# Kernel optimization log

Hardware: AMD Instinct MI355X
Metric: run time of the kernel (lower is better)

## Reference

```python
import jax, jax.numpy as jnp
import numpy as np

N_ENT, N_REL, N_TRIG, N_ARGS = 100000, 250000, 50000, 250000
ENT_DIM, REL_R, RTYPE_DIM, ROLE_DIM, REL_SIZE = 288, 256, 32, 256, 200
ARG_DIM = REL_R + RTYPE_DIM + ENT_DIM  # 576


def setup_inputs() -> dict:
    key = jax.random.key(0)
    ks = jax.random.split(key, 11)
    s_in = 1.0 / np.sqrt(ARG_DIM)
    return {
        "ent_embeds": jax.random.normal(ks[0], (N_ENT, ENT_DIM), jnp.float32),
        "rel_embeds": jax.random.normal(ks[1], (N_REL, REL_R), jnp.float32),
        "rtype_table": jax.random.normal(ks[2], (REL_SIZE + 1, RTYPE_DIM), jnp.float32),
        "W_in": jax.random.normal(ks[3], (ARG_DIM, ROLE_DIM), jnp.float32) * s_in,
        "W_out": jax.random.normal(ks[4], (ARG_DIM, ROLE_DIM), jnp.float32) * s_in,
        "rtype_ids": jax.random.randint(ks[5], (N_REL,), 0, REL_SIZE, jnp.int32),
        "trig_ent_id": jax.random.randint(ks[6], (N_TRIG,), 0, N_ENT, jnp.int32),
        "arg_trig": jax.random.randint(ks[7], (N_ARGS,), 0, N_TRIG, jnp.int32),
        "arg_rel": jax.random.randint(ks[8], (N_ARGS,), 0, N_REL, jnp.int32),
        "arg_ent": jax.random.randint(ks[9], (N_ARGS,), 0, N_ENT, jnp.int32),
        "arg_is_in": jax.random.randint(ks[10], (N_ARGS,), 0, 2, jnp.int32),
    }


def reference(ent_embeds, rel_embeds, rtype_table, W_in, W_out,
              rtype_ids, trig_ent_id, arg_trig, arg_rel, arg_ent, arg_is_in):
    # per-relation type embedding (rtype_embedding_layer)
    rt_embeds = rtype_table[rtype_ids]                       # [N_REL, RTYPE_DIM]
    # per-argument gather + concat (get_arg_embeds): [rel | rtype | arg-entity]
    x = jnp.concatenate([rel_embeds[arg_rel],
                         rt_embeds[arg_rel],
                         ent_embeds[arg_ent]], axis=-1)      # [N_ARGS, ARG_DIM]
    # in_arg_layer vs out_arg_layer selected per argument (io_ids membership)
    m = arg_is_in.astype(x.dtype)[:, None]
    y = (x * m) @ W_in + (x * (1.0 - m)) @ W_out             # [N_ARGS, ROLE_DIM]
    # sum-aggregate per trigger (torch.sum over stacked arg embeds)
    args_sum = jax.ops.segment_sum(y, arg_trig, num_segments=N_TRIG)
    # concat trigger embedding with aggregated args (event_representation)
    return jnp.concatenate([ent_embeds[trig_ent_id], args_sum], axis=-1)  # [N_TRIG, ENT_DIM+ROLE_DIM]
```

## Files before the change

### kernel.cpp

```cpp
#include <hip/hip_runtime.h>
#include <hip/hip_bf16.h>
#include <stdint.h>

#define N_ENT    100000
#define N_REL    250000
#define N_TRIG   50000
#define N_ARGS   250000
#define ENT_DIM  288
#define REL_R    256
#define RTYPE_DIM 32
#define ROLE_DIM 256
#define ARG_DIM  576
#define OUT_DIM  544

#define BM 64
#define BK 32
#define NSTEP (ARG_DIM / BK)
#define LDPK 584
#define CSP 258

typedef __attribute__((ext_vector_type(8))) short bf16x8;
typedef __attribute__((ext_vector_type(4))) short bf16x4;
typedef __attribute__((ext_vector_type(4))) float f32x4;

__device__ __forceinline__ short f2b(float f) {
    union { float f; uint32_t u; } v; v.f = f;
    uint32_t u = v.u;
    uint32_t r = (u + 0x7fffu + ((u >> 16) & 1u)) >> 16;
    return (short)r;
}

__global__ void __launch_bounds__(256)
k_init(const float* __restrict__ ent, const int* __restrict__ trig_ent,
       float* __restrict__ out)
{
    const int t    = blockIdx.x * 4 + (threadIdx.x >> 6);
    const int lane = threadIdx.x & 63;
    const int e    = trig_ent[t];
    const float4* src = (const float4*)(ent + (size_t)e * ENT_DIM);
    float4*       dst = (float4*)(out + (size_t)t * OUT_DIM);
    const float4 z = {0.f, 0.f, 0.f, 0.f};
    dst[lane] = src[lane];
    if (lane < 8) dst[64 + lane] = src[64 + lane];
    dst[72 + lane] = z;
}

__global__ void __launch_bounds__(256)
k_prep_hist(const float* __restrict__ W_in, const float* __restrict__ W_out,
            short* __restrict__ Wb,
            const int* __restrict__ arg_trig, int* __restrict__ cnt)
{
    const int idx = blockIdx.x * 256 + threadIdx.x;
    {
        const int w   = idx / (ARG_DIM * ROLE_DIM);
        const int rem = idx % (ARG_DIM * ROLE_DIM);
        const int k   = rem / ROLE_DIM;
        const int col = rem % ROLE_DIM;
        const float* src = (w == 0) ? W_in : W_out;
        Wb[((size_t)w * ROLE_DIM + col) * ARG_DIM + k] = f2b(src[k * ROLE_DIM + col]);
    }
    if (idx < N_ARGS) atomicAdd(&cnt[arg_trig[idx]], 1);
}

#define SCAN_T 1024
#define SCAN_B ((N_TRIG + SCAN_T - 1) / SCAN_T)

__global__ void __launch_bounds__(SCAN_T)
k_scan1(const int* __restrict__ cnt, int* __restrict__ off,
        int* __restrict__ bsum)
{
    __shared__ int buf[SCAN_T];
    const int tid = threadIdx.x;
    const int i   = blockIdx.x * SCAN_T + tid;
    int v = (i < N_TRIG) ? cnt[i] : 0;
    buf[tid] = v;
    __syncthreads();
#pragma unroll
    for (int o = 1; o < SCAN_T; o <<= 1) {
        int x = (tid >= o) ? buf[tid - o] : 0;
        __syncthreads();
        buf[tid] += x;
        __syncthreads();
    }
    if (i < N_TRIG) off[i] = buf[tid] - v;
    if (tid == SCAN_T - 1) bsum[blockIdx.x] = buf[tid];
}

__global__ void __launch_bounds__(SCAN_T)
k_scan3(int* __restrict__ off, const int* __restrict__ bsum)
{
    __shared__ int sh;
    if (threadIdx.x == 0) {
        int s = 0;
        for (int j = 0; j < (int)blockIdx.x; ++j) s += bsum[j];
        sh = s;
    }
    __syncthreads();
    const int i = blockIdx.x * SCAN_T + threadIdx.x;
    if (i < N_TRIG) off[i] += sh;
}

__global__ void __launch_bounds__(256)
k_scatter(const int* __restrict__ arg_trig, int* __restrict__ off,
          int* __restrict__ idx)
{
    const int a = blockIdx.x * 256 + threadIdx.x;
    if (a < N_ARGS) {
        const int p = atomicAdd(&off[arg_trig[a]], 1);
        idx[p] = a;
    }
}

__global__ void __launch_bounds__(512, 4)
k_gemm(const float* __restrict__ ent,  const float* __restrict__ rel,
       const float* __restrict__ rtab, const short* __restrict__ Wb,
       const int* __restrict__ rtype_ids, const int* __restrict__ arg_trig,
       const int* __restrict__ arg_rel,   const int* __restrict__ arg_ent,
       const int* __restrict__ arg_is_in, const int* __restrict__ idx,
       float* __restrict__ out)
{
    __shared__ alignas(16) short As[BM][LDPK];
    __shared__ int s_rel[BM], s_ent[BM], s_rt[BM], s_trig[BM], s_mask[BM];

    const int tid = threadIdx.x;
    const int a0  = blockIdx.x * BM;

    if (tid < BM) {
        int i     = a0 + tid;
        int valid = (i < N_ARGS);
        int a     = idx[valid ? i : (N_ARGS - 1)];
        int r     = arg_rel[a];
        s_rel[tid]  = r;
        s_ent[tid]  = arg_ent[a];
        s_rt[tid]   = rtype_ids[r];
        s_trig[tid] = valid ? arg_trig[a] : -1;
        s_mask[tid] = valid ? arg_is_in[a] : -1;
    }
    __syncthreads();

    const int lane  = tid & 63;
    const int wave  = tid >> 6;
    const int quad  = lane >> 4;
    const int l15   = lane & 15;
    const int nbase = wave * 32;

    const int srow = tid >> 3;
    const int skq  = (tid & 7) * 4;

    const float* p_rel = rel  + (size_t)s_rel[srow] * REL_R    + skq;
    const float* p_rt  = rtab + s_rt[srow] * RTYPE_DIM         + skq;
    const float* p_ent = ent  + (size_t)s_ent[srow] * ENT_DIM  + skq;

    {
        float4 t[9];
#pragma unroll
        for (int s = 0; s < 8; ++s) t[s] = *(const float4*)(p_rel + s * BK);
        t[8] = *(const float4*)p_rt;
#pragma unroll
        for (int s = 0; s < 9; ++s) {
            bf16x4 h;
            h[0] = f2b(t[s].x); h[1] = f2b(t[s].y);
            h[2] = f2b(t[s].z); h[3] = f2b(t[s].w);
            *(bf16x4*)&As[srow][s * BK + skq] = h;
        }
    }
    {
        float4 t[9];
#pragma unroll
        for (int s = 0; s < 9; ++s) t[s] = *(const float4*)(p_ent + s * BK);
#pragma unroll
        for (int s = 0; s < 9; ++s) {
            bf16x4 h;
            h[0] = f2b(t[s].x); h[1] = f2b(t[s].y);
            h[2] = f2b(t[s].z); h[3] = f2b(t[s].w);
            *(bf16x4*)&As[srow][(s + 9) * BK + skq] = h;
        }
    }

    int rowmask[4];
#pragma unroll
    for (int m = 0; m < 4; ++m) rowmask[m] = s_mask[m * 16 + l15];

    f32x4 acc[4][2];
#pragma unroll
    for (int m = 0; m < 4; ++m)
#pragma unroll
        for (int n = 0; n < 2; ++n) acc[m][n] = (f32x4){0.f, 0.f, 0.f, 0.f};

    const short* wbl = Wb + (size_t)(nbase + l15) * ARG_DIM + quad * 8;
    const bf16x8 zf = {0, 0, 0, 0, 0, 0, 0, 0};

    __syncthreads();

#pragma unroll
    for (int s = 0; s < NSTEP; ++s) {
        const short* bp = wbl + s * BK;
        const bf16x8 bi0 = *(const bf16x8*)(bp);
        const bf16x8 bi1 = *(const bf16x8*)(bp + 16 * ARG_DIM);
        const bf16x8 bo0 = *(const bf16x8*)(bp + (size_t)ROLE_DIM * ARG_DIM);
        const bf16x8 bo1 = *(const bf16x8*)(bp + (size_t)(ROLE_DIM + 16) * ARG_DIM);

        bf16x8 a[4];
#pragma unroll
        for (int m = 0; m < 4; ++m)
            a[m] = *(const bf16x8*)&As[m * 16 + l15][s * BK + quad * 8];

#pragma unroll
        for (int m = 0; m < 4; ++m) {
            const bf16x8 ain = (rowmask[m] == 1) ? a[m] : zf;
            const bf16x8 aot = (rowmask[m] == 0) ? a[m] : zf;
            acc[m][0] = __builtin_amdgcn_mfma_f32_16x16x32_bf16(ain, bi0, acc[m][0], 0, 0, 0);
            acc[m][0] = __builtin_amdgcn_mfma_f32_16x16x32_bf16(aot, bo0, acc[m][0], 0, 0, 0);
            acc[m][1] = __builtin_amdgcn_mfma_f32_16x16x32_bf16(ain, bi1, acc[m][1], 0, 0, 0);
            acc[m][1] = __builtin_amdgcn_mfma_f32_16x16x32_bf16(aot, bo1, acc[m][1], 0, 0, 0);
        }
    }

    __syncthreads();
    float (*Cs)[CSP] = (float(*)[CSP])&As[0][0];
#pragma unroll
    for (int m = 0; m < 4; ++m)
#pragma unroll
        for (int n = 0; n < 2; ++n)
#pragma unroll
            for (int r4 = 0; r4 < 4; ++r4)
                Cs[m * 16 + quad * 4 + r4][nbase + n * 16 + l15] = acc[m][n][r4];
    __syncthreads();

    {
        const int c    = tid & 255;
        const int half = tid >> 8;
        const int r0   = half * 32;
        const int rend = r0 + 32;

        int   runTrig  = s_trig[r0];
        int   runStart = r0;
        float sum      = 0.f;
        for (int r = r0; r < rend; ++r) {
            const int t = s_trig[r];
            if (t != runTrig) {
                if (runTrig >= 0) {
                    float* p = out + (size_t)runTrig * OUT_DIM + ENT_DIM + c;
                    if (runStart == r0) atomicAdd(p, sum);
                    else                *p = sum;
                }
                runTrig = t; runStart = r; sum = 0.f;
            }
            sum += Cs[r][c];
        }
        if (runTrig >= 0) {
            float* p = out + (size_t)runTrig * OUT_DIM + ENT_DIM + c;
            atomicAdd(p, sum);
        }
    }
}

extern "C" void kernel_launch(void* const* d_in, const int* in_sizes, int n_in,
                              void* d_out, int out_size, void* d_ws, size_t ws_size,
                              hipStream_t stream)
{
    const float* ent      = (const float*)d_in[0];
    const float* rel      = (const float*)d_in[1];
    const float* rtab     = (const float*)d_in[2];
    const float* W_in     = (const float*)d_in[3];
    const float* W_out    = (const float*)d_in[4];
    const int*  rtype_ids = (const int*)d_in[5];
    const int*  trig_ent  = (const int*)d_in[6];
    const int*  arg_trig  = (const int*)d_in[7];
    const int*  arg_rel   = (const int*)d_in[8];
    const int*  arg_ent   = (const int*)d_in[9];
    const int*  arg_is_in = (const int*)d_in[10];

    float* out = (float*)d_out;

    char* ws   = (char*)d_ws;
    short* Wb  = (short*)(ws);
    int*   cnt = (int*)(ws + 589824);
    int*   off = (int*)(ws + 789824);
    int*   bsum= (int*)(ws + 989824);
    int*   idx = (int*)(ws + 990080);

    hipMemsetAsync(cnt, 0, 200000, stream);

    hipLaunchKernelGGL(k_init, dim3(N_TRIG / 4), dim3(256), 0, stream,
                       ent, trig_ent, out);
    hipLaunchKernelGGL(k_prep_hist, dim3(2 * ARG_DIM * ROLE_DIM / 256), dim3(256),
                       0, stream, W_in, W_out, Wb, arg_trig, cnt);
    hipLaunchKernelGGL(k_scan1, dim3(SCAN_B), dim3(SCAN_T), 0, stream,
                       cnt, off, bsum);
    hipLaunchKernelGGL(k_scan3, dim3(SCAN_B), dim3(SCAN_T), 0, stream,
                       off, bsum);
    hipLaunchKernelGGL(k_scatter, dim3((N_ARGS + 255) / 256), dim3(256), 0,
                       stream, arg_trig, off, idx);
    hipLaunchKernelGGL(k_gemm, dim3((N_ARGS + BM - 1) / BM), dim3(512), 0, stream,
                       ent, rel, rtab, Wb,
                       rtype_ids, arg_trig, arg_rel, arg_ent, arg_is_in, idx, out);
}
```

Before: 755.4 us.

## Pre-convert embedding tables to bf16 before gathering into GEMM tiles

Adds a conversion kernel that writes bf16 copies of the relation, entity and rtype tables into workspace. The GEMM then gathers half-width rows with 16-byte loads instead of converting fp32 rows per tile. It also switches the init copy to nontemporal stores. The aim is to cut gather bandwidth and conversion work in the GEMM, at the cost of a full-table conversion pass on every call. The new path is used only when the workspace is large enough.

```diff
diff --git a/kernel.cpp b/kernel.cpp
--- a/kernel.cpp
+++ b/kernel.cpp
@@ -12,6 +12,7 @@
 #define ROLE_DIM 256
 #define ARG_DIM  576
 #define OUT_DIM  544
+#define REL_SIZE_PLUS1 201
 
 #define BM 64
 #define BK 32
@@ -19,6 +20,10 @@
 #define LDPK 584
 #define CSP 258
 
+#define RELB_STRIDE 256
+#define ENTB_STRIDE 320
+#define RTB_STRIDE  32
+
 typedef __attribute__((ext_vector_type(8))) short bf16x8;
 typedef __attribute__((ext_vector_type(4))) short bf16x4;
 typedef __attribute__((ext_vector_type(4))) float f32x4;
@@ -29,6 +34,12 @@
     uint32_t r = (u + 0x7fffu + ((u >> 16) & 1u)) >> 16;
     return (short)r;
 }
+__device__ __forceinline__ bf16x8 cvt8(float4 a, float4 b) {
+    bf16x8 h;
+    h[0] = f2b(a.x); h[1] = f2b(a.y); h[2] = f2b(a.z); h[3] = f2b(a.w);
+    h[4] = f2b(b.x); h[5] = f2b(b.y); h[6] = f2b(b.z); h[7] = f2b(b.w);
+    return h;
+}
 
 __global__ void __launch_bounds__(256)
 k_init(const float* __restrict__ ent, const int* __restrict__ trig_ent,
@@ -37,12 +48,13 @@
     const int t    = blockIdx.x * 4 + (threadIdx.x >> 6);
     const int lane = threadIdx.x & 63;
     const int e    = trig_ent[t];
-    const float4* src = (const float4*)(ent + (size_t)e * ENT_DIM);
-    float4*       dst = (float4*)(out + (size_t)t * OUT_DIM);
-    const float4 z = {0.f, 0.f, 0.f, 0.f};
-    dst[lane] = src[lane];
-    if (lane < 8) dst[64 + lane] = src[64 + lane];
-    dst[72 + lane] = z;
+    const f32x4* src = (const f32x4*)(ent + (size_t)e * ENT_DIM);
+    f32x4*       dst = (f32x4*)(out + (size_t)t * OUT_DIM);
+    const f32x4 z = {0.f, 0.f, 0.f, 0.f};
+    __builtin_nontemporal_store(src[lane], &dst[lane]);
+    if (lane < 8)
+        __builtin_nontemporal_store(src[64 + lane], &dst[64 + lane]);
+    __builtin_nontemporal_store(z, &dst[72 + lane]);
 }
 
 __global__ void __launch_bounds__(256)
@@ -62,6 +74,40 @@
     if (idx < N_ARGS) atomicAdd(&cnt[arg_trig[idx]], 1);
 }
 
+#define CONV_REL_BLOCKS 31250
+#define CONV_ENT_ELEMS  (N_ENT * ENT_DIM)
+#define CONV_ENT_BLOCKS 14063
+#define CONV_RT_BLOCKS  26
+#define CONV_BLOCKS (CONV_REL_BLOCKS + CONV_ENT_BLOCKS + CONV_RT_BLOCKS)
+
+__global__ void __launch_bounds__(256)
+k_conv(const float* __restrict__ rel, const float* __restrict__ ent,
+       const float* __restrict__ rtab,
+       short* __restrict__ relb, short* __restrict__ entb,
+       short* __restrict__ rtb)
+{
+    const int b = blockIdx.x;
+    if (b < CONV_REL_BLOCKS) {
+        const int i = (b * 256 + threadIdx.x) * 8;
+        float4 v0 = *(const float4*)(rel + i);
+        float4 v1 = *(const float4*)(rel + i + 4);
+        __builtin_nontemporal_store(cvt8(v0, v1), (bf16x8*)(relb + i));
+    } else if (b < CONV_REL_BLOCKS + CONV_ENT_BLOCKS) {
+        const int i = ((b - CONV_REL_BLOCKS) * 256 + threadIdx.x) * 8;
+        if (i < CONV_ENT_ELEMS) {
+            float4 v0 = *(const float4*)(ent + i);
+            float4 v1 = *(const float4*)(ent + i + 4);
+            const int row = i / ENT_DIM;
+            const int col = i - row * ENT_DIM;
+            __builtin_nontemporal_store(
+                cvt8(v0, v1), (bf16x8*)(entb + (size_t)row * ENTB_STRIDE + col));
+        }
+    } else {
+        const int i = (b - CONV_REL_BLOCKS - CONV_ENT_BLOCKS) * 256 + threadIdx.x;
+        if (i < (REL_SIZE_PLUS1 * RTYPE_DIM)) rtb[i] = f2b(rtab[i]);
+    }
+}
+
 #define SCAN_T 1024
 #define SCAN_B ((N_TRIG + SCAN_T - 1) / SCAN_T)
 
@@ -111,9 +157,12 @@
     }
 }
 
+template<int BF16TAB>
 __global__ void __launch_bounds__(512, 4)
 k_gemm(const float* __restrict__ ent,  const float* __restrict__ rel,
        const float* __restrict__ rtab, const short* __restrict__ Wb,
+       const short* __restrict__ relb, const short* __restrict__ entb,
+       const short* __restrict__ rtb,
        const int* __restrict__ rtype_ids, const int* __restrict__ arg_trig,
        const int* __restrict__ arg_rel,   const int* __restrict__ arg_ent,
        const int* __restrict__ arg_is_in, const int* __restrict__ idx,
@@ -145,35 +194,67 @@
     const int nbase = wave * 32;
 
     const int srow = tid >> 3;
-    const int skq  = (tid & 7) * 4;
-
-    const float* p_rel = rel  + (size_t)s_rel[srow] * REL_R    + skq;
-    const float* p_rt  = rtab + s_rt[srow] * RTYPE_DIM         + skq;
-    const float* p_ent = ent  + (size_t)s_ent[srow] * ENT_DIM  + skq;
-
-    {
-        float4 t[9];
-#pragma unroll
-        for (int s = 0; s < 8; ++s) t[s] = *(const float4*)(p_rel + s * BK);
-        t[8] = *(const float4*)p_rt;
-#pragma unroll
-        for (int s = 0; s < 9; ++s) {
-            bf16x4 h;
-            h[0] = f2b(t[s].x); h[1] = f2b(t[s].y);
-            h[2] = f2b(t[s].z); h[3] = f2b(t[s].w);
-            *(bf16x4*)&As[srow][s * BK + skq] = h;
-        }
-    }
-    {
-        float4 t[9];
-#pragma unroll
-        for (int s = 0; s < 9; ++s) t[s] = *(const float4*)(p_ent + s * BK);
-#pragma unroll
-        for (int s = 0; s < 9; ++s) {
-            bf16x4 h;
-            h[0] = f2b(t[s].x); h[1] = f2b(t[s].y);
-            h[2] = f2b(t[s].z); h[3] = f2b(t[s].w);
-            *(bf16x4*)&As[srow][(s + 9) * BK + skq] = h;
+    const int sub  = tid & 7;
+
+    if constexpr (BF16TAB) {
+        const short* q_rel = relb + (size_t)s_rel[srow] * RELB_STRIDE + sub * 8;
+        const short* q_ent = entb + (size_t)s_ent[srow] * ENTB_STRIDE + sub * 8;
+        const short* q_rt  = rtb  + s_rt[srow] * RTB_STRIDE + sub * 8;
+
+        bf16x8 r0 = *(const bf16x8*)(q_rel);
+        bf16x8 r1 = *(const bf16x8*)(q_rel + 64);
+        bf16x8 r2 = *(const bf16x8*)(q_rel + 128);
+        bf16x8 r3 = *(const bf16x8*)(q_rel + 192);
+        bf16x8 e0 = *(const bf16x8*)(q_ent);
+        bf16x8 e1 = *(const bf16x8*)(q_ent + 64);
+        bf16x8 e2 = *(const bf16x8*)(q_ent + 128);
+        bf16x8 e3 = *(const bf16x8*)(q_ent + 192);
+        bf16x8 rt4, e4;
+        if (sub < 4) {
+            rt4 = *(const bf16x8*)(q_rt);
+            e4  = *(const bf16x8*)(q_ent + 256);
+        }
+        *(bf16x8*)&As[srow][      sub * 8] = r0;
+        *(bf16x8*)&As[srow][ 64 + sub * 8] = r1;
+        *(bf16x8*)&As[srow][128 + sub * 8] = r2;
+        *(bf16x8*)&As[srow][192 + sub * 8] = r3;
+        *(bf16x8*)&As[srow][288 + sub * 8] = e0;
+        *(bf16x8*)&As[srow][352 + sub * 8] = e1;
+        *(bf16x8*)&As[srow][416 + sub * 8] = e2;
+        *(bf16x8*)&As[srow][480 + sub * 8] = e3;
+        if (sub < 4) {
+            *(bf16x8*)&As[srow][256 + sub * 8] = rt4;
+            *(bf16x8*)&As[srow][544 + sub * 8] = e4;
+        }
+    } else {
+        const int skq = sub * 4;
+        const float* p_rel = rel  + (size_t)s_rel[srow] * REL_R    + skq;
+        const float* p_rt  = rtab + s_rt[srow] * RTYPE_DIM         + skq;
+        const float* p_ent = ent  + (size_t)s_ent[srow] * ENT_DIM  + skq;
+        {
+            float4 t[9];
+#pragma unroll
+            for (int s = 0; s < 8; ++s) t[s] = *(const float4*)(p_rel + s * BK);
+            t[8] = *(const float4*)p_rt;
+#pragma unroll
+            for (int s = 0; s < 9; ++s) {
+                bf16x4 h;
+                h[0] = f2b(t[s].x); h[1] = f2b(t[s].y);
+                h[2] = f2b(t[s].z); h[3] = f2b(t[s].w);
+                *(bf16x4*)&As[srow][s * BK + skq] = h;
+            }
+        }
+        {
+            float4 t[9];
+#pragma unroll
+            for (int s = 0; s < 9; ++s) t[s] = *(const float4*)(p_ent + s * BK);
+#pragma unroll
+            for (int s = 0; s < 9; ++s) {
+                bf16x4 h;
+                h[0] = f2b(t[s].x); h[1] = f2b(t[s].y);
+                h[2] = f2b(t[s].z); h[3] = f2b(t[s].w);
+                *(bf16x4*)&As[srow][(s + 9) * BK + skq] = h;
+            }
         }
     }
 
@@ -279,20 +360,33 @@
     int*   off = (int*)(ws + 789824);
     int*   bsum= (int*)(ws + 989824);
     int*   idx = (int*)(ws + 990080);
-
-    hipMemsetAsync(cnt, 0, 200000, stream);
+    short* rtb = (short*)(ws + 1990080);
+    short* relb= (short*)(ws + 2002944);
+    short* entb= (short*)(ws + 130002944ULL);
+
+    const bool bf16tabs = (ws_size >= 194002944ULL);
+
+    (void)hipMemsetAsync(cnt, 0, 200000, stream);
 
     hipLaunchKernelGGL(k_init, dim3(N_TRIG / 4), dim3(256), 0, stream,
                        ent, trig_ent, out);
     hipLaunchKernelGGL(k_prep_hist, dim3(2 * ARG_DIM * ROLE_DIM / 256), dim3(256),
                        0, stream, W_in, W_out, Wb, arg_trig, cnt);
+    if (bf16tabs)
+        hipLaunchKernelGGL(k_conv, dim3(CONV_BLOCKS), dim3(256), 0, stream,
+                           rel, ent, rtab, relb, entb, rtb);
     hipLaunchKernelGGL(k_scan1, dim3(SCAN_B), dim3(SCAN_T), 0, stream,
                        cnt, off, bsum);
     hipLaunchKernelGGL(k_scan3, dim3(SCAN_B), dim3(SCAN_T), 0, stream,
                        off, bsum);
     hipLaunchKernelGGL(k_scatter, dim3((N_ARGS + 255) / 256), dim3(256), 0,
                        stream, arg_trig, off, idx);
-    hipLaunchKernelGGL(k_gemm, dim3((N_ARGS + BM - 1) / BM), dim3(512), 0, stream,
-                       ent, rel, rtab, Wb,
-                       rtype_ids, arg_trig, arg_rel, arg_ent, arg_is_in, idx, out);
-}
+    if (bf16tabs)
+        hipLaunchKernelGGL(k_gemm<1>, dim3((N_ARGS + BM - 1) / BM), dim3(512), 0,
+                           stream, ent, rel, rtab, Wb, relb, entb, rtb,
+                           rtype_ids, arg_trig, arg_rel, arg_ent, arg_is_in, idx, out);
+    else
+        hipLaunchKernelGGL(k_gemm<0>, dim3((N_ARGS + BM - 1) / BM), dim3(512), 0,
+                           stream, ent, rel, rtab, Wb, relb, entb, rtb,
+                           rtype_ids, arg_trig, arg_rel, arg_ent, arg_is_in, idx, out);
+}
```

Measured after the change: 836.4 us. 10.7% more time.
